# Kernel optimization log

Measured on AMD Instinct MI355X. Metric: run time of the kernel, lower is better.

The kernel has to match this reference:

```python
import jax, jax.numpy as jnp
import numpy as np

NUM_FEATURE = 512
HIDDEN = 256
NUM_CLASSES = 10
L1 = 1e-4
ALPHA = 1e-3
BATCH = 65536


def setup_inputs() -> dict:
    key = jax.random.key(0)
    k = jax.random.split(key, 6)
    x = jax.random.normal(k[0], (BATCH, NUM_FEATURE), dtype=jnp.float32)
    y = jax.random.randint(k[1], (BATCH,), 0, NUM_CLASSES, dtype=jnp.int32)
    fc0 = jax.random.normal(k[2], (NUM_FEATURE, 512), dtype=jnp.float32) / NUM_FEATURE
    fc1 = jax.random.normal(k[3], (NUM_FEATURE, 512), dtype=jnp.float32) / NUM_FEATURE
    w = jax.random.normal(k[4], (NUM_FEATURE, HIDDEN), dtype=jnp.float32) / NUM_FEATURE
    w1 = jax.random.normal(k[5], (HIDDEN, NUM_CLASSES), dtype=jnp.float32) / HIDDEN
    return {"x": x, "y": y, "fc0": fc0, "fc1": fc1, "w": w, "w1": w1}


def reference(x, y, fc0, fc1, w, w1):
    # sigmoid-gated MLP block with residual
    x1 = x @ fc0                                   # [B, 512]
    x2 = jax.nn.relu(x @ fc1)                      # [B, 512]
    x4 = x + (1.0 + jax.nn.sigmoid(x1)) * x2       # [B, 512] residual

    # head (Dropout(p=0.0) is identity)
    logits = jax.nn.relu(x4 @ w) @ w1              # [B, 10]
    pred = jnp.argmax(logits, axis=1)

    # cross-entropy (mean over batch)
    logp = jax.nn.log_softmax(logits, axis=-1)
    ce = -jnp.mean(jnp.take_along_axis(logp, y[:, None].astype(jnp.int32), axis=1))

    # L1 penalty on all weight matrices
    l1_pen = L1 * (jnp.abs(w1).sum() + jnp.abs(w).sum()
                   + jnp.abs(fc0).sum() + jnp.abs(fc1).sum())

    # per-class variance: sum_i ||mean_{y_i} - x4_i||^2, vectorized via segment sums
    counts = jax.ops.segment_sum(jnp.ones((x4.shape[0],), jnp.float32), y,
                                 num_segments=NUM_CLASSES)
    sums = jax.ops.segment_sum(x4, y, num_segments=NUM_CLASSES)   # [10, 512]
    means = sums / jnp.maximum(counts, 1.0)[:, None]
    var_loss = jnp.sum(jnp.square(means[y] - x4))

    loss = ce + l1_pen + ALPHA * var_loss
    acc = jnp.mean((pred.astype(jnp.int32) == y.astype(jnp.int32)).astype(jnp.float32))
    return (loss, acc)
```

## Files before the change

kernel.cpp:

```cpp
#include <hip/hip_runtime.h>
#include <stdint.h>

#define BATCH 65536
#define FDIM 512
#define HDIM 256
#define NC 10
#define NREP 16

typedef short short8 __attribute__((ext_vector_type(8)));
typedef float f32x4 __attribute__((ext_vector_type(4)));

#define OFF_FC0T   ((size_t)0)
#define OFF_FC1T   (OFF_FC0T + (size_t)512*512*2)
#define OFF_WT     (OFF_FC1T + (size_t)512*512*2)
#define OFF_XT     (OFF_WT   + (size_t)256*512*2)
#define OFF_X4T    (OFF_XT   + (size_t)BATCH*512*2)
#define OFF_ACC    (OFF_X4T  + (size_t)BATCH*512*2)
#define SCAL_SUMSQ 0
#define SCAL_CE    16
#define SCAL_ACC   32
#define SCAL_L1    48
#define SCAL_CTR   64
#define SCAL_N     128
#define CNT_OFF    SCAL_N
#define GSUM_OFF   (SCAL_N + NREP*16)
#define ACC_FLOATS (GSUM_OFF + NREP*5120)
#define OFF_W1T    (OFF_ACC + (size_t)ACC_FLOATS*4)

#define GLL(g,l) __builtin_amdgcn_global_load_lds((const __attribute__((address_space(1))) void*)(g), (__attribute__((address_space(3))) void*)(l), 16, 0, 0)

__device__ __forceinline__ unsigned short f2b(float f){
  unsigned u = __float_as_uint(f);
  u += 0x7FFFu + ((u >> 16) & 1u);
  return (unsigned short)(u >> 16);
}
__device__ __forceinline__ float b2f(unsigned short h){
  return __uint_as_float(((unsigned)h) << 16);
}
__device__ __forceinline__ unsigned pk2b(float f0, float f1){
  unsigned u0 = __float_as_uint(f0) + 0x8000u;
  unsigned u1 = __float_as_uint(f1) + 0x8000u;
  return __builtin_amdgcn_perm(u1, u0, 0x07060302u);
}
__device__ __forceinline__ float ald(const float* p){
  return __hip_atomic_load(p, __ATOMIC_RELAXED, __HIP_MEMORY_SCOPE_AGENT);
}

__global__ __launch_bounds__(256) void k_setup(
    const float* __restrict__ x,   const float* __restrict__ fc0,
    const float* __restrict__ fc1, const float* __restrict__ w,
    const float* __restrict__ w1,  const int* __restrict__ y,
    unsigned short* __restrict__ xT,   unsigned short* __restrict__ fc0T,
    unsigned short* __restrict__ fc1T, unsigned short* __restrict__ wT,
    unsigned short* __restrict__ w1T,  float* __restrict__ accb)
{
  int blk = blockIdx.x, t = threadIdx.x;
  if (blk < 2048){
    __shared__ __align__(16) unsigned short xls[16*520];
    int wv = t >> 6, l = t & 63;
    #pragma unroll 1
    for (int it = 0; it < 2; ++it){
      int I = blk*2 + it;
      #pragma unroll
      for (int rr = 0; rr < 4; ++rr){
        int row = wv*4 + rr;
        const float* src = x + ((size_t)(I*16 + row))*FDIM + l*8;
        float4 v0 = *(const float4*)src;
        float4 v1 = *(const float4*)(src + 4);
        unsigned o[4];
        o[0] = pk2b(v0.x, v0.y); o[1] = pk2b(v0.z, v0.w);
        o[2] = pk2b(v1.x, v1.y); o[3] = pk2b(v1.z, v1.w);
        *(short8*)&xls[row*520 + l*8] = *(short8*)o;
      }
      __syncthreads();
      #pragma unroll
      for (int cc = 0; cc < 4; ++cc){
        int C = cc*4 + wv;
        short8 v = *(const short8*)&xls[(l & 15)*520 + C*32 + (l >> 4)*8];
        *(short8*)&xT[(((size_t)I*16 + C) << 9) + l*8] = v;
      }
      __syncthreads();
    }
    return;
  }
  if (blk < 2384){
    int i = (blk - 2048)*256 + t;
    float l1v = 0.f;
    if (i < 32768){
      int n4 = i&15, m = (i>>4)&3, C = (i>>6)&15, J = i>>10;
      int n = J*16+n4, k8 = C*4+m;
      unsigned short o[8];
      #pragma unroll
      for (int j=0;j<8;++j){ float v = fc0[(size_t)(k8*8+j)*512 + n]; o[j]=f2b(v); l1v += fabsf(v); }
      *(short8*)&fc0T[(size_t)(J*16+C)*512 + (i&63)*8] = *(short8*)o;
    } else if (i < 65536){
      int j0 = i - 32768;
      int n4 = j0&15, m = (j0>>4)&3, C = (j0>>6)&15, J = j0>>10;
      int n = J*16+n4, k8 = C*4+m;
      unsigned short o[8];
      #pragma unroll
      for (int j=0;j<8;++j){ float v = fc1[(size_t)(k8*8+j)*512 + n]; o[j]=f2b(v); l1v += fabsf(v); }
      *(short8*)&fc1T[(size_t)(J*16+C)*512 + (j0&63)*8] = *(short8*)o;
    } else if (i < 81920){
      int j0 = i - 65536;
      int n4 = j0&15, m = (j0>>4)&3, C = (j0>>6)&15, J = j0>>10;
      int n = J*16+n4, k8 = C*4+m;
      unsigned short o[8];
      #pragma unroll
      for (int j=0;j<8;++j){ float v = w[(size_t)(k8*8+j)*256 + n]; o[j]=f2b(v); l1v += fabsf(v); }
      *(short8*)&wT[(size_t)(J*16+C)*512 + (j0&63)*8] = *(short8*)o;
    } else if (i < 86016){
      int j0 = i - 81920;
      int C = j0 >> 9, l = (j0 >> 3) & 63, e = j0 & 7;
      int n = l & 15, k = C*32 + (l>>4)*8 + e;
      float v = (n < NC) ? w1[k*NC + n] : 0.f;
      w1T[C*512 + l*8 + e] = f2b(v);
      if (n < NC) l1v = fabsf(v);
    }
    for (int off = 32; off; off >>= 1) l1v += __shfl_down(l1v, off);
    if ((t & 63) == 0 && l1v != 0.f)
      atomicAdd(&accb[SCAL_L1 + (blk & (NREP-1))], l1v);
    return;
  }
  if (blk < 2465){
    int base = (blk - 2384)*1024;
    #pragma unroll
    for (int j=0;j<4;++j){
      int idx = base + j*256 + t;
      if (idx < ACC_FLOATS && (idx < CNT_OFF || idx >= CNT_OFF + NREP*16))
        accb[idx] = 0.f;
    }
    return;
  }
  {
    __shared__ float cntS[16];
    int b = blk - 2465;
    if (t < 16) cntS[t] = 0.f;
    __syncthreads();
    int base = b*4096;
    for (int i = t; i < 4096; i += 256) atomicAdd(&cntS[y[base+i]], 1.f);
    __syncthreads();
    if (t < 16) accb[CNT_OFF + b*16 + t] = cntS[t];
  }
}


#define BARRIER() __builtin_amdgcn_s_barrier()
#define LGKM0() do{ asm volatile("s_waitcnt lgkmcnt(0)" ::: "memory"); \
                    __builtin_amdgcn_sched_barrier(0); }while(0)

#define RA(AB, C) do{                                                         \
  _Pragma("unroll") for (int m_=0;m_<8;++m_)                                  \
    a[m_] = *(const short8*)((AB) + (((wr*8+m_)*2 + (C))<<10) + lane*16);     \
}while(0)

#define RB(AB, MAT, C) do{                                                    \
  _Pragma("unroll") for (int n_=0;n_<2;++n_)                                  \
    bb[n_] = *(const short8*)((AB) + 32768 + (MAT)*16384 +                    \
                              (((wc*2+n_)*2 + (C))<<10) + lane*16);           \
}while(0)

#define MM16(ACC) do{                                                         \
  __builtin_amdgcn_s_setprio(1);                                              \
  _Pragma("unroll") for (int n_=0;n_<2;++n_)                                  \
  _Pragma("unroll") for (int m_=0;m_<8;++m_)                                  \
    ACC[m_][n_] = __builtin_amdgcn_mfma_f32_16x16x32_bf16(a[m_], bb[n_], ACC[m_][n_], 0,0,0); \
  __builtin_amdgcn_s_setprio(0);                                              \
}while(0)

#define SA(KT, C) do{                                                         \
  char* d_ = ldsd + (((KT)&1) ? 65536 : 0);                                   \
  _Pragma("unroll") for (int r_=0;r_<2;++r_){                                 \
    int I_ = wv + r_*8;                                                       \
    GLL(xb + (((size_t)((rowblk*16 + I_)*16 + (KT)*2 + (C))) << 10) + lane*16,\
        d_ + ((I_*2 + (C)) << 10) + lane*16);                                 \
  } }while(0)

#define SB(KT, C) do{                                                         \
  char* d_ = ldsd + (((KT)&1) ? 65536 : 0) + 32768;                           \
  GLL(b0b + (((size_t)((colblk*8 + wv)*16 + (KT)*2 + (C))) << 10) + lane*16,  \
      d_ + ((wv*2 + (C)) << 10) + lane*16);                                   \
  GLL(b1b + (((size_t)((colblk*8 + wv)*16 + (KT)*2 + (C))) << 10) + lane*16,  \
      d_ + 16384 + ((wv*2 + (C)) << 10) + lane*16);                           \
}while(0)

#define KLOOP() do{                                                           \
  SA(0,0); SB(0,0); SA(0,1); SB(0,1); SA(1,0); SB(1,0); SA(1,1);              \
  asm volatile("s_waitcnt vmcnt(6)" ::: "memory");                            \
  __builtin_amdgcn_sched_barrier(0);                                          \
  BARRIER();                                                                  \
  _Pragma("unroll")                                                           \
  for (int i = 0; i < 4; ++i){                                                \
    int kt0 = 2*i, kt1 = 2*i+1;                                               \
    char* Ab0 = ldsd + ((kt0 & 1) ? 65536 : 0);                               \
    char* Ab1 = ldsd + ((kt1 & 1) ? 65536 : 0);                               \
    RA(Ab0, 0); RB(Ab0, 0, 0);                                                \
    SB(kt1, 1);                                                               \
    BARRIER(); LGKM0(); MM16(acc1);                                           \
    BARRIER();                                                                \
    RB(Ab0, 1, 0);                                                            \
    if (i < 3) SA(kt0+2, 0);                                                  \
    BARRIER(); LGKM0(); MM16(acc2);                                           \
    BARRIER();                                                                \
    RA(Ab0, 1); RB(Ab0, 0, 1);                                                \
    if (i < 3) SB(kt0+2, 0);                                                  \
    BARRIER(); LGKM0(); MM16(acc1);                                           \
    BARRIER();                                                                \
    RB(Ab0, 1, 1);                                                            \
    if (i < 3) SA(kt0+2, 1);                                                  \
    BARRIER(); LGKM0(); MM16(acc2);                                           \
    if (i < 3) { asm volatile("s_waitcnt vmcnt(6)" ::: "memory"); }           \
    else       { asm volatile("s_waitcnt vmcnt(0)" ::: "memory"); }           \
    __builtin_amdgcn_sched_barrier(0);                                        \
    BARRIER();                                                                \
    RA(Ab1, 0); RB(Ab1, 0, 0);                                                \
    if (i < 3) SB(kt0+2, 1);                                                  \
    BARRIER(); LGKM0(); MM16(acc1);                                           \
    BARRIER();                                                                \
    RB(Ab1, 1, 0);                                                            \
    if (i < 3) SA(kt1+2, 0);                                                  \
    BARRIER(); LGKM0(); MM16(acc2);                                           \
    BARRIER();                                                                \
    RA(Ab1, 1); RB(Ab1, 0, 1);                                                \
    if (i < 3) SB(kt1+2, 0);                                                  \
    BARRIER(); LGKM0(); MM16(acc1);                                           \
    BARRIER();                                                                \
    RB(Ab1, 1, 1);                                                            \
    if (i < 3) SA(kt1+2, 1);                                                  \
    BARRIER(); LGKM0(); MM16(acc2);                                           \
    if (i < 3) { asm volatile("s_waitcnt vmcnt(6)" ::: "memory");             \
                 __builtin_amdgcn_sched_barrier(0); }                         \
    BARRIER();                                                                \
  }                                                                           \
}while(0)

__global__ __launch_bounds__(512, 2) void k_gemm12(
    const unsigned short* __restrict__ xT,
    const unsigned short* __restrict__ fc0T,
    const unsigned short* __restrict__ fc1T,
    const int* __restrict__ y,
    unsigned short* __restrict__ x4T,
    float* __restrict__ accb)
{
  extern __shared__ __align__(16) char ldsd[];
  float* scal = accb;
  float* gsum = accb + GSUM_OFF;

  int blk = blockIdx.x;
  int wg = (blk & 7)*128 + (blk >> 3);
  int rowblk = wg >> 2;
  int colblk = wg & 3;

  int t = threadIdx.x;
  int wv = t >> 6, lane = t & 63, ln = lane & 15, quad = lane >> 4;
  int wr = wv >> 2, wc = wv & 3;

  const char* xb  = (const char*)xT;
  const char* b0b = (const char*)fc0T;
  const char* b1b = (const char*)fc1T;

  const f32x4 zv = {0.f,0.f,0.f,0.f};
  f32x4 acc1[8][2], acc2[8][2];
  #pragma unroll
  for (int m=0;m<8;++m){ acc1[m][0]=zv; acc1[m][1]=zv; acc2[m][0]=zv; acc2[m][1]=zv; }

  short8 a[8], bb[2];

  KLOOP();

  {
    int Cres = colblk*4 + wc;
    #pragma unroll
    for (int i = 0; i < 8; ++i){
      GLL(xb + (((size_t)((rowblk*16 + wr*8 + i)*16 + Cres)) << 10) + lane*16,
          ldsd + ((wv*8 + i) << 10) + lane*16);
    }
    asm volatile("s_waitcnt vmcnt(0)" ::: "memory");
  }
  __syncthreads();

  unsigned short* resU = (unsigned short*)ldsd;
  unsigned short* x4U  = (unsigned short*)(ldsd + 65536);
  float sumsq = 0.f;
  #pragma unroll
  for (int m = 0; m < 8; ++m){
    #pragma unroll
    for (int n = 0; n < 2; ++n){
      #pragma unroll
      for (int r = 0; r < 4; ++r){
        int slot = (quad*4 + r) | ((n*2 + (ln>>3)) << 4);
        int idx = ((wv*8 + m) << 9) + slot*8 + (ln & 7);
        float xv  = b2f(resU[idx]);
        float x1v = acc1[m][n][r];
        float x2v = fmaxf(acc2[m][n][r], 0.f);
        float gate = 1.f + 1.f/(1.f + __expf(-x1v));
        float x4v = fmaf(gate, x2v, xv);
        unsigned short ub = f2b(x4v);
        float fq = b2f(ub);
        sumsq = fmaf(fq, fq, sumsq);
        x4U[idx] = ub;
        acc1[m][n][r] = fq;
      }
    }
  }
  for (int off = 32; off; off >>= 1) sumsq += __shfl_down(sumsq, off);
  __syncthreads();

  float cs[NC][2];
  #pragma unroll
  for (int c=0;c<NC;++c){ cs[c][0]=0.f; cs[c][1]=0.f; }
  {
    const int* yrow = y + rowblk*256 + wr*128;
    #pragma unroll
    for (int m = 0; m < 8; ++m){
      int yv[4];
      #pragma unroll
      for (int r = 0; r < 4; ++r) yv[r] = yrow[m*16 + quad*4 + r];
      #pragma unroll
      for (int r = 0; r < 4; ++r){
        float v0 = acc1[m][0][r], v1 = acc1[m][1][r];
        #pragma unroll
        for (int c = 0; c < NC; ++c){
          bool msk = (yv[r] == c);
          cs[c][0] += msk ? v0 : 0.f;
          cs[c][1] += msk ? v1 : 0.f;
        }
      }
    }
  }
  #pragma unroll
  for (int c = 0; c < NC; ++c)
    #pragma unroll
    for (int n = 0; n < 2; ++n){
      cs[c][n] += __shfl_xor(cs[c][n], 16);
      cs[c][n] += __shfl_xor(cs[c][n], 32);
    }
  if (lane < 16){
    size_t gb = (size_t)(blk & (NREP-1))*5120 + colblk*128 + wc*32 + ln;
    #pragma unroll
    for (int c = 0; c < NC; ++c){
      atomicAdd(&gsum[gb + c*512],      cs[c][0]);
      atomicAdd(&gsum[gb + c*512 + 16], cs[c][1]);
    }
  }

  float* red = (float*)ldsd;
  if (lane == 0) red[wv] = sumsq;
  __syncthreads();
  if (t == 0){
    float s = 0.f;
    #pragma unroll
    for (int i=0;i<8;++i) s += red[i];
    atomicAdd(&scal[SCAL_SUMSQ + (blk & (NREP-1))], s);
  }
  #pragma unroll
  for (int r = 0; r < 2; ++r){
    int o = r*512 + t;
    int tile = o >> 6, off16 = o & 63;
    int wvp = tile >> 3, i = tile & 7;
    size_t Ig = (size_t)rowblk*16 + (wvp>>2)*8 + i;
    int Cg = colblk*4 + (wvp & 3);
    *(short8*)&x4T[((Ig*16 + Cg) << 9) + off16*8] =
      *(const short8*)&x4U[(tile << 9) + off16*8];
  }
}

__global__ __launch_bounds__(512, 2) void k_gemm3_head(
    const unsigned short* __restrict__ x4T,
    const unsigned short* __restrict__ wT,
    const unsigned short* __restrict__ w1T,
    const int* __restrict__ y,
    float* __restrict__ accb,
    float* __restrict__ out)
{
  extern __shared__ __align__(16) char ldsd[];
  __shared__ float redc[8], reda[8];
  __shared__ int lastB;

  float* scal = accb;

  int blk = blockIdx.x;
  int rowblk = blk;
  const int colblk = 0;

  int t = threadIdx.x;
  int wv = t >> 6, lane = t & 63, ln = lane & 15, quad = lane >> 4;
  int wr = wv >> 2, wc = wv & 3;
  int rep = (blk ^ (blk >> 4)) & (NREP-1);

  const char* xb  = (const char*)x4T;
  const char* b0b = (const char*)wT;
  const char* b1b = (const char*)wT + (size_t)128*1024;

  const f32x4 zv = {0.f,0.f,0.f,0.f};
  f32x4 acc1[8][2], acc2[8][2];
  #pragma unroll
  for (int m=0;m<8;++m){ acc1[m][0]=zv; acc1[m][1]=zv; acc2[m][0]=zv; acc2[m][1]=zv; }

  short8 a[8], bb[2];

  KLOOP();

  short8 bw1[8];
  #pragma unroll
  for (int Ck = 0; Ck < 8; ++Ck)
    bw1[Ck] = *(const short8*)&w1T[Ck*512 + lane*8];

  unsigned short* transH = (unsigned short*)ldsd;
  #pragma unroll
  for (int m = 0; m < 8; ++m){
    #pragma unroll
    for (int n = 0; n < 2; ++n){
      #pragma unroll
      for (int r = 0; r < 4; ++r){
        int slot = (quad*4 + r) | ((n*2 + (ln>>3)) << 4);
        int e = ln & 7;
        int IhA = wr*8 + m;
        transH[((IhA*8 + wc)     << 9) + slot*8 + e] = f2b(fmaxf(acc1[m][n][r], 0.f));
        transH[((IhA*8 + 4 + wc) << 9) + slot*8 + e] = f2b(fmaxf(acc2[m][n][r], 0.f));
      }
    }
  }
  __syncthreads();

  f32x4 alog[2] = {zv, zv};
  #pragma unroll
  for (int ih = 0; ih < 2; ++ih){
    int Ih = wv*2 + ih;
    #pragma unroll
    for (int Ck = 0; Ck < 8; ++Ck){
      short8 af = *(const short8*)&transH[((Ih*8 + Ck) << 9) + lane*8];
      alog[ih] = __builtin_amdgcn_mfma_f32_16x16x32_bf16(af, bw1[Ck], alog[ih], 0,0,0);
    }
  }

  float ce_l = 0.f, acc_l = 0.f;
  #pragma unroll
  for (int ih = 0; ih < 2; ++ih){
    #pragma unroll
    for (int r = 0; r < 4; ++r){
      int grow = blk*256 + (wv*2 + ih)*16 + quad*4 + r;
      int yv = y[grow];
      float lg = (ln < NC) ? alog[ih][r] : -1e30f;
      float m = lg; int mi = ln;
      #pragma unroll
      for (int mk = 1; mk < 16; mk <<= 1){
        float om = __shfl_xor(m, mk); int oi = __shfl_xor(mi, mk);
        if (om > m || (om == m && oi < mi)){ m = om; mi = oi; }
      }
      float e  = (ln < NC) ? __expf(lg - m) : 0.f;
      float sy = (ln == yv) ? lg : 0.f;
      #pragma unroll
      for (int mk = 1; mk < 16; mk <<= 1){ e += __shfl_xor(e, mk); sy += __shfl_xor(sy, mk); }
      float lse = m + __logf(e);
      if (ln == 0){ ce_l += (lse - sy); acc_l += (mi == yv) ? 1.f : 0.f; }
    }
  }
  ce_l  += __shfl_down(ce_l, 16);  acc_l += __shfl_down(acc_l, 16);
  ce_l  += __shfl_down(ce_l, 32);  acc_l += __shfl_down(acc_l, 32);
  if (lane == 0){ redc[wv] = ce_l; reda[wv] = acc_l; }
  __syncthreads();
  if (t == 0){
    float c = 0.f, aa = 0.f;
    #pragma unroll
    for (int i=0;i<8;++i){ c += redc[i]; aa += reda[i]; }
    atomicAdd(&scal[SCAL_CE  + rep], c);
    atomicAdd(&scal[SCAL_ACC + rep], aa);
    __threadfence();
    int prev = atomicAdd((int*)(scal + SCAL_CTR), 1);
    lastB = (prev == (int)gridDim.x - 1);
  }
  __syncthreads();
  if (!lastB) return;

  {
    const float* gsum = accb + GSUM_OFF;
    const float* gcnt = accb + CNT_OFF;
    float contrib = 0.f;
    for (int idx = t; idx < 5120; idx += 512){
      float S = 0.f;
      #pragma unroll
      for (int r = 0; r < NREP; ++r) S += ald(&gsum[(size_t)r*5120 + idx]);
      int c = idx >> 9;
      float cnt = 0.f;
      #pragma unroll
      for (int r = 0; r < NREP; ++r) cnt += ald(&gcnt[r*16 + c]);
      contrib += S*S / fmaxf(cnt, 1.f);
    }
    for (int off = 32; off; off >>= 1) contrib += __shfl_down(contrib, off);
    __syncthreads();
    if (lane == 0) redc[wv] = contrib;
    __syncthreads();
    if (t == 0){
      float var2 = 0.f;
      #pragma unroll
      for (int i=0;i<8;++i) var2 += redc[i];
      float sumsq=0.f, ce=0.f, accv=0.f, l1=0.f;
      for (int r=0;r<NREP;++r){
        sumsq += ald(&scal[SCAL_SUMSQ+r]);
        ce    += ald(&scal[SCAL_CE+r]);
        accv  += ald(&scal[SCAL_ACC+r]);
        l1    += ald(&scal[SCAL_L1+r]);
      }
      float var_loss = sumsq - var2;
      out[0] = ce/(float)BATCH + 1e-4f*l1 + 1e-3f*var_loss;
      out[1] = accv/(float)BATCH;
    }
  }
}

extern "C" void kernel_launch(void* const* d_in, const int* in_sizes, int n_in,
                              void* d_out, int out_size, void* d_ws, size_t ws_size,
                              hipStream_t stream){
  (void)in_sizes; (void)n_in; (void)out_size; (void)ws_size;
  const float* x   = (const float*)d_in[0];
  const int*   y   = (const int*)d_in[1];
  const float* fc0 = (const float*)d_in[2];
  const float* fc1 = (const float*)d_in[3];
  const float* w   = (const float*)d_in[4];
  const float* w1  = (const float*)d_in[5];
  char* ws = (char*)d_ws;
  unsigned short* fc0T = (unsigned short*)(ws + OFF_FC0T);
  unsigned short* fc1T = (unsigned short*)(ws + OFF_FC1T);
  unsigned short* wT   = (unsigned short*)(ws + OFF_WT);
  unsigned short* xT   = (unsigned short*)(ws + OFF_XT);
  unsigned short* x4T  = (unsigned short*)(ws + OFF_X4T);
  unsigned short* w1T  = (unsigned short*)(ws + OFF_W1T);
  float* accb = (float*)(ws + OFF_ACC);

  static bool once = [](){
    hipFuncSetAttribute((const void*)k_gemm12,
                        hipFuncAttributeMaxDynamicSharedMemorySize, 131072);
    hipFuncSetAttribute((const void*)k_gemm3_head,
                        hipFuncAttributeMaxDynamicSharedMemorySize, 131072);
    return true;
  }();
  (void)once;

  k_setup<<<2481, 256, 0, stream>>>(x, fc0, fc1, w, w1, y, xT, fc0T, fc1T, wT, w1T, accb);
  k_gemm12<<<1024, 512, 131072, stream>>>(xT, fc0T, fc1T, y, x4T, accb);
  k_gemm3_head<<<256, 512, 131072, stream>>>(x4T, wT, w1T, y, accb, (float*)d_out);
}
```

Baseline: 359.8 us.

## Halve gemm12 row tile and use simple double-buffered K loop for occupancy

Rewrites the fused fc0/fc1 GEMM kernel to use 128-row tiles instead of 256, doubling the grid to 2048 blocks and cutting dynamic LDS from 128 KB to 64 KB so more blocks can be resident. The hand-scheduled KLOOP pipeline is replaced by a plain double-buffered loop that prefetches one K-slice per iteration. The aim is more parallelism and better latency hiding through occupancy. The cost is less operand reuse per block, more global traffic for the weights, and a full barrier with a vmcnt(0) wait every iteration.

```diff
diff --git a/kernel.cpp b/kernel.cpp
--- a/kernel.cpp
+++ b/kernel.cpp
@@ -144,6 +144,172 @@
   }
 }
 
+__global__ __launch_bounds__(512, 4) void k_gemm12(
+    const unsigned short* __restrict__ xT,
+    const unsigned short* __restrict__ fc0T,
+    const unsigned short* __restrict__ fc1T,
+    const int* __restrict__ y,
+    unsigned short* __restrict__ x4T,
+    float* __restrict__ accb)
+{
+  extern __shared__ __align__(16) char ldsd[];
+  float* scal = accb;
+  float* gsum = accb + GSUM_OFF;
+
+  int blk = blockIdx.x;
+  int wg = (blk & 7)*256 + (blk >> 3);
+  int rowblk = wg >> 2;
+  int colblk = wg & 3;
+
+  int t = threadIdx.x;
+  int wv = t >> 6, lane = t & 63, ln = lane & 15, quad = lane >> 4;
+  int wr = wv >> 2, wc = wv & 3;
+
+  const char* xb  = (const char*)xT;
+  const char* b0b = (const char*)fc0T;
+  const char* b1b = (const char*)fc1T;
+
+  const f32x4 zv = {0.f,0.f,0.f,0.f};
+  f32x4 acc1[4][2], acc2[4][2];
+  #pragma unroll
+  for (int m=0;m<4;++m){ acc1[m][0]=zv; acc1[m][1]=zv; acc2[m][0]=zv; acc2[m][1]=zv; }
+
+  short8 a[4], b0r[2], b1r[2];
+
+  GLL(xb  + (((size_t)((rowblk*8+wv)*16 + 0)) << 10) + lane*16, ldsd +         (wv<<10) + lane*16);
+  GLL(b0b + (((size_t)((colblk*8+wv)*16 + 0)) << 10) + lane*16, ldsd +  8192 + (wv<<10) + lane*16);
+  GLL(b1b + (((size_t)((colblk*8+wv)*16 + 0)) << 10) + lane*16, ldsd + 16384 + (wv<<10) + lane*16);
+  asm volatile("s_waitcnt vmcnt(0)" ::: "memory");
+  __builtin_amdgcn_sched_barrier(0);
+  __builtin_amdgcn_s_barrier();
+
+  #pragma unroll
+  for (int kt = 0; kt < 16; ++kt){
+    char* cur = ldsd + ((kt & 1) ? 24576 : 0);
+    char* nxt = ldsd + ((kt & 1) ? 0 : 24576);
+    if (kt < 15){
+      GLL(xb  + (((size_t)((rowblk*8+wv)*16 + kt+1)) << 10) + lane*16, nxt +         (wv<<10) + lane*16);
+      GLL(b0b + (((size_t)((colblk*8+wv)*16 + kt+1)) << 10) + lane*16, nxt +  8192 + (wv<<10) + lane*16);
+      GLL(b1b + (((size_t)((colblk*8+wv)*16 + kt+1)) << 10) + lane*16, nxt + 16384 + (wv<<10) + lane*16);
+    }
+    #pragma unroll
+    for (int m=0;m<4;++m)
+      a[m] = *(const short8*)(cur + ((wr*4+m)<<10) + lane*16);
+    #pragma unroll
+    for (int n=0;n<2;++n){
+      b0r[n] = *(const short8*)(cur +  8192 + ((wc*2+n)<<10) + lane*16);
+      b1r[n] = *(const short8*)(cur + 16384 + ((wc*2+n)<<10) + lane*16);
+    }
+    asm volatile("s_waitcnt lgkmcnt(0)" ::: "memory");
+    __builtin_amdgcn_sched_barrier(0);
+    __builtin_amdgcn_s_setprio(1);
+    #pragma unroll
+    for (int n=0;n<2;++n)
+      #pragma unroll
+      for (int m=0;m<4;++m){
+        acc1[m][n] = __builtin_amdgcn_mfma_f32_16x16x32_bf16(a[m], b0r[n], acc1[m][n], 0,0,0);
+        acc2[m][n] = __builtin_amdgcn_mfma_f32_16x16x32_bf16(a[m], b1r[n], acc2[m][n], 0,0,0);
+      }
+    __builtin_amdgcn_s_setprio(0);
+    if (kt < 15){ asm volatile("s_waitcnt vmcnt(0)" ::: "memory"); }
+    __builtin_amdgcn_sched_barrier(0);
+    __builtin_amdgcn_s_barrier();
+  }
+
+  #pragma unroll
+  for (int c = 0; c < 4; ++c){
+    GLL(xb + (((size_t)((rowblk*8+wv)*16 + colblk*4 + c)) << 10) + lane*16,
+        ldsd + ((wv*4 + c) << 10) + lane*16);
+  }
+  asm volatile("s_waitcnt vmcnt(0)" ::: "memory");
+  __syncthreads();
+
+  unsigned short* resU = (unsigned short*)ldsd;
+  unsigned short* x4U  = (unsigned short*)(ldsd + 32768);
+  float sumsq = 0.f;
+  #pragma unroll
+  for (int m = 0; m < 4; ++m){
+    #pragma unroll
+    for (int n = 0; n < 2; ++n){
+      #pragma unroll
+      for (int r = 0; r < 4; ++r){
+        int slot = (quad*4 + r) | ((n*2 + (ln>>3)) << 4);
+        int idx = (((wr*4 + m)*4 + wc) << 9) + slot*8 + (ln & 7);
+        float xv  = b2f(resU[idx]);
+        float x1v = acc1[m][n][r];
+        float x2v = fmaxf(acc2[m][n][r], 0.f);
+        float gate = 1.f + 1.f/(1.f + __expf(-x1v));
+        float x4v = fmaf(gate, x2v, xv);
+        unsigned short ub = f2b(x4v);
+        float fq = b2f(ub);
+        sumsq = fmaf(fq, fq, sumsq);
+        x4U[idx] = ub;
+        acc1[m][n][r] = fq;
+      }
+    }
+  }
+  for (int off = 32; off; off >>= 1) sumsq += __shfl_down(sumsq, off);
+  __syncthreads();
+
+  float cs[NC][2];
+  #pragma unroll
+  for (int c=0;c<NC;++c){ cs[c][0]=0.f; cs[c][1]=0.f; }
+  {
+    const int* yrow = y + rowblk*128 + wr*64;
+    #pragma unroll
+    for (int m = 0; m < 4; ++m){
+      int yv[4];
+      #pragma unroll
+      for (int r = 0; r < 4; ++r) yv[r] = yrow[m*16 + quad*4 + r];
+      #pragma unroll
+      for (int r = 0; r < 4; ++r){
+        float v0 = acc1[m][0][r], v1 = acc1[m][1][r];
+        #pragma unroll
+        for (int c = 0; c < NC; ++c){
+          bool msk = (yv[r] == c);
+          cs[c][0] += msk ? v0 : 0.f;
+          cs[c][1] += msk ? v1 : 0.f;
+        }
+      }
+    }
+  }
+  #pragma unroll
+  for (int c = 0; c < NC; ++c)
+    #pragma unroll
+    for (int n = 0; n < 2; ++n){
+      cs[c][n] += __shfl_xor(cs[c][n], 16);
+      cs[c][n] += __shfl_xor(cs[c][n], 32);
+    }
+  if (lane < 16){
+    size_t gb = (size_t)(blk & (NREP-1))*5120 + colblk*128 + wc*32 + ln;
+    #pragma unroll
+    for (int c = 0; c < NC; ++c){
+      atomicAdd(&gsum[gb + c*512],      cs[c][0]);
+      atomicAdd(&gsum[gb + c*512 + 16], cs[c][1]);
+    }
+  }
+
+  float* red = (float*)ldsd;
+  if (lane == 0) red[wv] = sumsq;
+  __syncthreads();
+  if (t == 0){
+    float s = 0.f;
+    #pragma unroll
+    for (int i=0;i<8;++i) s += red[i];
+    atomicAdd(&scal[SCAL_SUMSQ + (blk & (NREP-1))], s);
+  }
+  #pragma unroll
+  for (int r = 0; r < 4; ++r){
+    int o = r*512 + t;
+    int tile = o >> 6, off16 = o & 63;
+    int Il = tile >> 2, Cl = tile & 3;
+    size_t Ig = (size_t)rowblk*8 + Il;
+    int Cg = colblk*4 + Cl;
+    *(short8*)&x4T[((Ig*16 + Cg) << 9) + off16*8] =
+      *(const short8*)&x4U[(tile << 9) + off16*8];
+  }
+}
+
 
 #define BARRIER() __builtin_amdgcn_s_barrier()
 #define LGKM0() do{ asm volatile("s_waitcnt lgkmcnt(0)" ::: "memory"); \
@@ -233,137 +399,6 @@
     BARRIER();                                                                \
   }                                                                           \
 }while(0)
-
-__global__ __launch_bounds__(512, 2) void k_gemm12(
-    const unsigned short* __restrict__ xT,
-    const unsigned short* __restrict__ fc0T,
-    const unsigned short* __restrict__ fc1T,
-    const int* __restrict__ y,
-    unsigned short* __restrict__ x4T,
-    float* __restrict__ accb)
-{
-  extern __shared__ __align__(16) char ldsd[];
-  float* scal = accb;
-  float* gsum = accb + GSUM_OFF;
-
-  int blk = blockIdx.x;
-  int wg = (blk & 7)*128 + (blk >> 3);
-  int rowblk = wg >> 2;
-  int colblk = wg & 3;
-
-  int t = threadIdx.x;
-  int wv = t >> 6, lane = t & 63, ln = lane & 15, quad = lane >> 4;
-  int wr = wv >> 2, wc = wv & 3;
-
-  const char* xb  = (const char*)xT;
-  const char* b0b = (const char*)fc0T;
-  const char* b1b = (const char*)fc1T;
-
-  const f32x4 zv = {0.f,0.f,0.f,0.f};
-  f32x4 acc1[8][2], acc2[8][2];
-  #pragma unroll
-  for (int m=0;m<8;++m){ acc1[m][0]=zv; acc1[m][1]=zv; acc2[m][0]=zv; acc2[m][1]=zv; }
-
-  short8 a[8], bb[2];
-
-  KLOOP();
-
-  {
-    int Cres = colblk*4 + wc;
-    #pragma unroll
-    for (int i = 0; i < 8; ++i){
-      GLL(xb + (((size_t)((rowblk*16 + wr*8 + i)*16 + Cres)) << 10) + lane*16,
-          ldsd + ((wv*8 + i) << 10) + lane*16);
-    }
-    asm volatile("s_waitcnt vmcnt(0)" ::: "memory");
-  }
-  __syncthreads();
-
-  unsigned short* resU = (unsigned short*)ldsd;
-  unsigned short* x4U  = (unsigned short*)(ldsd + 65536);
-  float sumsq = 0.f;
-  #pragma unroll
-  for (int m = 0; m < 8; ++m){
-    #pragma unroll
-    for (int n = 0; n < 2; ++n){
-      #pragma unroll
-      for (int r = 0; r < 4; ++r){
-        int slot = (quad*4 + r) | ((n*2 + (ln>>3)) << 4);
-        int idx = ((wv*8 + m) << 9) + slot*8 + (ln & 7);
-        float xv  = b2f(resU[idx]);
-        float x1v = acc1[m][n][r];
-        float x2v = fmaxf(acc2[m][n][r], 0.f);
-        float gate = 1.f + 1.f/(1.f + __expf(-x1v));
-        float x4v = fmaf(gate, x2v, xv);
-        unsigned short ub = f2b(x4v);
-        float fq = b2f(ub);
-        sumsq = fmaf(fq, fq, sumsq);
-        x4U[idx] = ub;
-        acc1[m][n][r] = fq;
-      }
-    }
-  }
-  for (int off = 32; off; off >>= 1) sumsq += __shfl_down(sumsq, off);
-  __syncthreads();
-
-  float cs[NC][2];
-  #pragma unroll
-  for (int c=0;c<NC;++c){ cs[c][0]=0.f; cs[c][1]=0.f; }
-  {
-    const int* yrow = y + rowblk*256 + wr*128;
-    #pragma unroll
-    for (int m = 0; m < 8; ++m){
-      int yv[4];
-      #pragma unroll
-      for (int r = 0; r < 4; ++r) yv[r] = yrow[m*16 + quad*4 + r];
-      #pragma unroll
-      for (int r = 0; r < 4; ++r){
-        float v0 = acc1[m][0][r], v1 = acc1[m][1][r];
-        #pragma unroll
-        for (int c = 0; c < NC; ++c){
-          bool msk = (yv[r] == c);
-          cs[c][0] += msk ? v0 : 0.f;
-          cs[c][1] += msk ? v1 : 0.f;
-        }
-      }
-    }
-  }
-  #pragma unroll
-  for (int c = 0; c < NC; ++c)
-    #pragma unroll
-    for (int n = 0; n < 2; ++n){
-      cs[c][n] += __shfl_xor(cs[c][n], 16);
-      cs[c][n] += __shfl_xor(cs[c][n], 32);
-    }
-  if (lane < 16){
-    size_t gb = (size_t)(blk & (NREP-1))*5120 + colblk*128 + wc*32 + ln;
-    #pragma unroll
-    for (int c = 0; c < NC; ++c){
-      atomicAdd(&gsum[gb + c*512],      cs[c][0]);
-      atomicAdd(&gsum[gb + c*512 + 16], cs[c][1]);
-    }
-  }
-
-  float* red = (float*)ldsd;
-  if (lane == 0) red[wv] = sumsq;
-  __syncthreads();
-  if (t == 0){
-    float s = 0.f;
-    #pragma unroll
-    for (int i=0;i<8;++i) s += red[i];
-    atomicAdd(&scal[SCAL_SUMSQ + (blk & (NREP-1))], s);
-  }
-  #pragma unroll
-  for (int r = 0; r < 2; ++r){
-    int o = r*512 + t;
-    int tile = o >> 6, off16 = o & 63;
-    int wvp = tile >> 3, i = tile & 7;
-    size_t Ig = (size_t)rowblk*16 + (wvp>>2)*8 + i;
-    int Cg = colblk*4 + (wvp & 3);
-    *(short8*)&x4T[((Ig*16 + Cg) << 9) + off16*8] =
-      *(const short8*)&x4U[(tile << 9) + off16*8];
-  }
-}
 
 __global__ __launch_bounds__(512, 2) void k_gemm3_head(
     const unsigned short* __restrict__ x4T,
@@ -530,7 +565,7 @@
 
   static bool once = [](){
     hipFuncSetAttribute((const void*)k_gemm12,
-                        hipFuncAttributeMaxDynamicSharedMemorySize, 131072);
+                        hipFuncAttributeMaxDynamicSharedMemorySize, 65536);
     hipFuncSetAttribute((const void*)k_gemm3_head,
                         hipFuncAttributeMaxDynamicSharedMemorySize, 131072);
     return true;
@@ -538,6 +573,6 @@
   (void)once;
 
   k_setup<<<2481, 256, 0, stream>>>(x, fc0, fc1, w, w1, y, xT, fc0T, fc1T, wT, w1T, accb);
-  k_gemm12<<<1024, 512, 131072, stream>>>(xT, fc0T, fc1T, y, x4T, accb);
+  k_gemm12<<<2048, 512, 65536, stream>>>(xT, fc0T, fc1T, y, x4T, accb);
   k_gemm3_head<<<256, 512, 131072, stream>>>(x4T, wT, w1T, y, accb, (float*)d_out);
 }
```

New measurement: 352.2 us (median of 2 runs). -2.1%, faster.
